# Performance work log

Hardware: AMD Instinct MI355X
Metric: run time of the kernel (lower is better)

The kernel has to match this reference:

```python
import jax, jax.numpy as jnp
import numpy as np

N = 50000
E = 800000
F_IN, F_HID, F_OUT = 128, 64, 40


def setup_inputs() -> dict:
    key = jax.random.key(0)
    ks = jax.random.split(key, 8)
    x = jax.random.normal(ks[0], (N, F_IN), dtype=jnp.float32)
    edge_index = jax.random.randint(ks[1], (2, E), 0, N, dtype=jnp.int64)
    # Glorot-style init like PyG GCNConv.lin; stored as [in, out]
    def glorot(k, fi, fo):
        s = jnp.sqrt(6.0 / (fi + fo)).astype(jnp.float32)
        return jax.random.uniform(k, (fi, fo), jnp.float32, -s, s)
    W1 = glorot(ks[2], F_IN, F_HID)
    b1 = jnp.zeros((F_HID,), jnp.float32)
    W2 = glorot(ks[3], F_HID, F_HID)
    b2 = jnp.zeros((F_HID,), jnp.float32)
    W3 = glorot(ks[4], F_HID, F_OUT)
    b3 = jnp.zeros((F_OUT,), jnp.float32)
    return {"x": x, "edge_index": edge_index, "W1": W1, "b1": b1,
            "W2": W2, "b2": b2, "W3": W3, "b3": b3}


def _prep_edges(edge_index):
    # add self-loops, compute symmetric GCN normalization (as PyG gcn_norm)
    loops = jnp.arange(N, dtype=edge_index.dtype)
    src = jnp.concatenate([edge_index[0], loops])
    dst = jnp.concatenate([edge_index[1], loops])
    deg = jax.ops.segment_sum(jnp.ones_like(dst, dtype=jnp.float32), dst,
                              num_segments=N)
    dinv = jnp.where(deg > 0, jax.lax.rsqrt(deg), 0.0)
    norm = dinv[src] * dinv[dst]  # [E+N]
    return src, dst, norm


def _gcn_conv(x, W, b, src, dst, norm):
    h = x @ W                                  # [N, out] dense projection
    msg = h[src] * norm[:, None]               # gather + scale, [E+N, out]
    out = jax.ops.segment_sum(msg, dst, num_segments=N)  # scatter-add
    return out + b


def reference(x, edge_index, W1, b1, W2, b2, W3, b3):
    src, dst, norm = _prep_edges(edge_index)
    h = jax.nn.relu(_gcn_conv(x, W1, b1, src, dst, norm))
    h = jax.nn.relu(_gcn_conv(h, W2, b2, src, dst, norm))
    return _gcn_conv(h, W3, b3, src, dst, norm)
```

## Files before the change

### kernel.cpp

```cpp
#include <hip/hip_runtime.h>
#include <hip/hip_fp16.h>
#include <math.h>

#define NN 50000
#define EE 800000
#define FIN 128
#define FHID 64
#define FOUT 40

#define BSH  6
#define NBKT ((NN + 63) >> 6)
#define CAP  1600
#define KBBLK 128
#define CHK  (EE / KBBLK)


__global__ void k_detect(const unsigned int* __restrict__ w, int* __restrict__ flag,
                         int* __restrict__ gcur) {
    int t = threadIdx.x;
    if (t < NBKT) gcur[t] = t * CAP;
    if (t == 0) *flag = 1;
    __syncthreads();
    unsigned v = w[2 * t + 1];
    unsigned long long b = __ballot(v != 0);
    if (b && (t & 63) == 0) atomicAnd(flag, 0);
}


__global__ __launch_bounds__(256) void k_bucket(const unsigned int* __restrict__ w,
                                                const int* __restrict__ flag,
                                                int* __restrict__ gcur,
                                                unsigned int* __restrict__ BKT) {
    __shared__ int hist[NBKT], rsv[NBKT], lcur[NBKT];
    const int tid = threadIdx.x;
    for (int i = tid; i < NBKT; i += 256) { hist[i] = 0; lcur[i] = 0; }
    __syncthreads();
    const bool f64 = (*flag) != 0;
    const int e0 = blockIdx.x * CHK, e1 = e0 + CHK;

    for (int e = e0 + tid; e < e1; e += 256) {
        unsigned d = f64 ? w[2 * (EE + e)] : w[EE + e];
        atomicAdd(&hist[d >> BSH], 1);
    }
    __syncthreads();
    for (int i = tid; i < NBKT; i += 256) {
        int h = hist[i];
        rsv[i] = h ? atomicAdd(&gcur[i], h) : 0;
    }
    __syncthreads();
    for (int e = e0 + tid; e < e1; e += 256) {
        unsigned s, d;
        if (f64) { s = w[2 * e]; d = w[2 * (EE + e)]; }
        else     { s = w[e];     d = w[EE + e]; }
        unsigned b = d >> BSH;
        int idx = atomicAdd(&lcur[b], 1);
        BKT[rsv[b] + idx] = (d << 16) | s;
    }
}

__global__ __launch_bounds__(256) void k_fine(const unsigned int* __restrict__ BKT,
                                              const int* __restrict__ gcur,
                                              int* __restrict__ off,
                                              float* __restrict__ dinv,
                                              unsigned short* __restrict__ ebuf) {
    __shared__ unsigned st[CAP];
    __shared__ int h[64], sc[64], lc[64];
    __shared__ int red[4];
    const int tid  = threadIdx.x;
    const int lane = tid & 63;
    const int wid  = tid >> 6;
    const int b    = blockIdx.x;

    int partial = 0;
    for (int i = tid; i < b; i += 256) partial += gcur[i] - i * CAP;
#pragma unroll
    for (int o = 1; o < 64; o <<= 1) partial += __shfl_xor(partial, o, 64);
    if (lane == 0) red[wid] = partial;
    if (tid < 64) { h[tid] = 0; lc[tid] = 0; }
    __syncthreads();
    const int bb = red[0] + red[1] + red[2] + red[3];

    int cnt = gcur[b] - b * CAP;
    if (cnt > CAP) cnt = CAP;
    for (int i = tid; i < cnt; i += 256) {
        unsigned p = BKT[b * CAP + i];
        st[i] = p;
        atomicAdd(&h[(p >> 16) & 63], 1);
    }
    __syncthreads();
    if (tid < 64) {
        int v = h[tid];
        int incl = v;
#pragma unroll
        for (int o = 1; o < 64; o <<= 1) {
            int u = __shfl_up(incl, o, 64);
            if (tid >= o) incl += u;
        }
        sc[tid] = incl - v;
        int n = (b << BSH) + tid;
        if (n < NN) {
            off[n]  = bb + sc[tid];
            dinv[n] = 1.0f / sqrtf((float)(v + 1));
        }
    }
    if (b == 0 && tid == 64) off[NN] = EE;
    __syncthreads();
    for (int i = tid; i < cnt; i += 256) {
        unsigned p = st[i];
        int l = (p >> 16) & 63;
        int idx = atomicAdd(&lc[l], 1);
        ebuf[bb + sc[l] + idx] = (unsigned short)(p & 0xffffu);
    }
}


__global__ __launch_bounds__(256) void k_gemm1(const float* __restrict__ X,
                                               const float* __restrict__ W,
                                               const float* __restrict__ dinv,
                                               unsigned short* __restrict__ Ph) {
    constexpr int K = FIN, ROWS = 16, XP = K + 4;
    __shared__ float Ws[K * 64];
    __shared__ float Xs[ROWS * XP];
    const int tid  = threadIdx.x;
    const int row0 = blockIdx.x * ROWS;
    const int row_end = (NN - row0 < ROWS) ? (NN - row0) : ROWS;

    for (int i = tid; i < K * 16; i += 256)
        ((float4*)Ws)[i] = ((const float4*)W)[i];
    for (int i = tid; i < row_end * (K / 4); i += 256) {
        int r = i / (K / 4), c = i % (K / 4);
        float4 v = ((const float4*)X)[(size_t)(row0 + r) * (K / 4) + c];
        *(float4*)&Xs[r * XP + 4 * c] = v;
    }
    __syncthreads();

    const int r  = tid >> 4;
    const int cg = tid & 15;
    const int grow = row0 + r;
    if (r >= row_end) return;

    float a0 = 0.f, a1 = 0.f, a2 = 0.f, a3 = 0.f;
#pragma unroll 4
    for (int k = 0; k < K; k++) {
        float xv = Xs[r * XP + k];
        float4 wv = *(const float4*)&Ws[k * 64 + cg * 4];
        a0 = fmaf(xv, wv.x, a0);
        a1 = fmaf(xv, wv.y, a1);
        a2 = fmaf(xv, wv.z, a2);
        a3 = fmaf(xv, wv.w, a3);
    }
    float dv = dinv[grow];
    ushort4 o;
    o.x = __half_as_ushort(__float2half_rn(a0 * dv));
    o.y = __half_as_ushort(__float2half_rn(a1 * dv));
    o.z = __half_as_ushort(__float2half_rn(a2 * dv));
    o.w = __half_as_ushort(__float2half_rn(a3 * dv));
    *(ushort4*)&Ph[(size_t)grow * 64 + cg * 4] = o;
}


__device__ __forceinline__ void acc_h(float4& acc, uint2 u) {
    __half2 h01 = *reinterpret_cast<const __half2*>(&u.x);
    __half2 h23 = *reinterpret_cast<const __half2*>(&u.y);
    acc.x += __low2float(h01);
    acc.y += __high2float(h01);
    acc.z += __low2float(h23);
    acc.w += __high2float(h23);
}

__device__ __forceinline__ float4 gather_row_sum(const uint2* __restrict__ Pu,
                                                 const unsigned short* __restrict__ ebuf,
                                                 int node, int s, int e, int g, int q) {
    float4 acc = {0.f, 0.f, 0.f, 0.f};
    if (g == 0) acc_h(acc, Pu[(size_t)node * 16 + q]);
    int i = s;
    for (; i + 15 < e; i += 16) {
        int c0 = ebuf[i + g], c1 = ebuf[i + g + 4], c2 = ebuf[i + g + 8], c3 = ebuf[i + g + 12];
        uint2 u0 = Pu[(size_t)c0 * 16 + q];
        uint2 u1 = Pu[(size_t)c1 * 16 + q];
        uint2 u2 = Pu[(size_t)c2 * 16 + q];
        uint2 u3 = Pu[(size_t)c3 * 16 + q];
        acc_h(acc, u0); acc_h(acc, u1); acc_h(acc, u2); acc_h(acc, u3);
    }
    if (i < e) {
        int j0 = i + g, j1 = i + g + 4, j2 = i + g + 8, j3 = i + g + 12;
        uint2 u0 = Pu[(size_t)ebuf[j0 < e ? j0 : e - 1] * 16 + q];
        uint2 u1 = Pu[(size_t)ebuf[j1 < e ? j1 : e - 1] * 16 + q];
        uint2 u2 = Pu[(size_t)ebuf[j2 < e ? j2 : e - 1] * 16 + q];
        uint2 u3 = Pu[(size_t)ebuf[j3 < e ? j3 : e - 1] * 16 + q];
        if (j0 < e) acc_h(acc, u0);
        if (j1 < e) acc_h(acc, u1);
        if (j2 < e) acc_h(acc, u2);
        if (j3 < e) acc_h(acc, u3);
    }
#pragma unroll
    for (int o = 16; o <= 32; o <<= 1) {
        acc.x += __shfl_xor(acc.x, o, 64);
        acc.y += __shfl_xor(acc.y, o, 64);
        acc.z += __shfl_xor(acc.z, o, 64);
        acc.w += __shfl_xor(acc.w, o, 64);
    }
    return acc;
}


__global__ __launch_bounds__(256) void k_agg1(const uint2* __restrict__ Pu,
                                              const int* __restrict__ off,
                                              const unsigned short* __restrict__ ebuf,
                                              const float* __restrict__ dinv,
                                              const float4* __restrict__ bias4,
                                              unsigned short* __restrict__ HA) {
    const int gid  = blockIdx.x * blockDim.x + threadIdx.x;
    const int node = gid >> 6;
    const int lane = threadIdx.x & 63;
    if (node >= NN) return;
    const int g = lane >> 4, q = lane & 15;
    float4 acc = gather_row_sum(Pu, ebuf, node, off[node], off[node + 1], g, q);
    if (lane < 16) {
        float dv = dinv[node];
        float4 b = bias4[q];
        float4 v;
        v.x = fmaxf(fmaf(acc.x, dv, b.x), 0.f) * dv;
        v.y = fmaxf(fmaf(acc.y, dv, b.y), 0.f) * dv;
        v.z = fmaxf(fmaf(acc.z, dv, b.z), 0.f) * dv;
        v.w = fmaxf(fmaf(acc.w, dv, b.w), 0.f) * dv;
        ushort4 o;
        o.x = __half_as_ushort(__float2half_rn(v.x));
        o.y = __half_as_ushort(__float2half_rn(v.y));
        o.z = __half_as_ushort(__float2half_rn(v.z));
        o.w = __half_as_ushort(__float2half_rn(v.w));
        ((ushort4*)HA)[(size_t)node * 16 + q] = o;
    }
}


template <int MOUT, bool OUTF16>
__global__ __launch_bounds__(256) void k_fuse(const uint2* __restrict__ Hu,
                                              const float* __restrict__ W,
                                              const int* __restrict__ off,
                                              const unsigned short* __restrict__ ebuf,
                                              const float* __restrict__ dinv,
                                              const float* __restrict__ bias,
                                              void* __restrict__ outv) {
    __shared__ float Ws[64 * MOUT];
    __shared__ float aggL[4 * 64];
    const int tid  = threadIdx.x;
    const int lane = tid & 63;
    const int wv   = tid >> 6;
    const int g = lane >> 4, q = lane & 15;

    for (int i = tid; i < 64 * MOUT / 4; i += 256)
        ((float4*)Ws)[i] = ((const float4*)W)[i];
    __syncthreads();

    const float bv = (lane < MOUT) ? bias[lane] : 0.f;
    const int n0 = blockIdx.x * 16 + wv * 4;

#pragma unroll 1
    for (int j = 0; j < 4; j++) {
        const int node = n0 + j;
        float4 acc = gather_row_sum(Hu, ebuf, node, off[node], off[node + 1], g, q);
        const float dv = dinv[node];
        if (lane < 16) {
            float4 t;
            t.x = acc.x * dv; t.y = acc.y * dv; t.z = acc.z * dv; t.w = acc.w * dv;
            *(float4*)&aggL[wv * 64 + q * 4] = t;
        }
        if (lane < MOUT) {
            float o = 0.f;
#pragma unroll 8
            for (int k = 0; k < 64; k++)
                o = fmaf(aggL[wv * 64 + k], Ws[k * MOUT + lane], o);
            float v = o + bv;
            if constexpr (OUTF16) {
                v = fmaxf(v, 0.f);
                ((unsigned short*)outv)[(size_t)node * 64 + lane] =
                    __half_as_ushort(__float2half_rn(v * dv));
            } else {
                ((float*)outv)[(size_t)node * MOUT + lane] = v;
            }
        }
    }
}


static inline size_t alignup(size_t x) { return (x + 255) & ~(size_t)255; }

extern "C" void kernel_launch(void* const* d_in, const int* in_sizes, int n_in,
                              void* d_out, int out_size, void* d_ws, size_t ws_size,
                              hipStream_t stream) {
    const float*        x  = (const float*)d_in[0];
    const unsigned int* ew = (const unsigned int*)d_in[1];
    const float*        W1 = (const float*)d_in[2];
    const float*        b1 = (const float*)d_in[3];
    const float*        W2 = (const float*)d_in[4];
    const float*        b2 = (const float*)d_in[5];
    const float*        W3 = (const float*)d_in[6];
    const float*        b3 = (const float*)d_in[7];

    char* w = (char*)d_ws;
    int*            flag = (int*)w;            w += alignup(4);
    int*            gcur = (int*)w;            w += alignup(NBKT * 4);
    int*            off  = (int*)w;            w += alignup((NN + 1) * 4);
    float*          dinv = (float*)w;          w += alignup(NN * 4);
    unsigned int*   BKT  = (unsigned int*)w;   w += alignup((size_t)NBKT * CAP * 4);
    unsigned short* ebuf = (unsigned short*)w; w += alignup(EE * 2);
    unsigned short* Ph   = (unsigned short*)w; w += alignup((size_t)NN * 64 * 2);
    unsigned short* HA   = (unsigned short*)w; w += alignup((size_t)NN * 64 * 2);
    unsigned short* HB   = (unsigned short*)w; w += alignup((size_t)NN * 64 * 2);

    const int BA = (NN * 64) / 256;
    const int BG = (NN + 15) / 16;

    k_detect<<<1, 1024, 0, stream>>>(ew, flag, gcur);
    k_bucket<<<KBBLK, 256, 0, stream>>>(ew, flag, gcur, BKT);
    k_fine<<<NBKT, 256, 0, stream>>>(BKT, gcur, off, dinv, ebuf);

    k_gemm1<<<BG, 256, 0, stream>>>(x, W1, dinv, Ph);
    k_agg1<<<BA, 256, 0, stream>>>((const uint2*)Ph, off, ebuf, dinv,
                                   (const float4*)b1, HA);

    k_fuse<FHID, true><<<BG, 256, 0, stream>>>((const uint2*)HA, W2, off, ebuf,
                                               dinv, b2, HB);

    k_fuse<FOUT, false><<<BG, 256, 0, stream>>>((const uint2*)HB, W3, off, ebuf,
                                                dinv, b3, d_out);
}
```

Before: 220.6 us.

## Widen gather loads to 16-byte rows and use one wave per node in fused layers

```diff
diff --git a/kernel.cpp b/kernel.cpp
--- a/kernel.cpp
+++ b/kernel.cpp
@@ -159,126 +159,134 @@
 }
 
 
-__device__ __forceinline__ void acc_h(float4& acc, uint2 u) {
+__device__ __forceinline__ void acc_h8(float4& A, float4& B, uint4 u) {
     __half2 h01 = *reinterpret_cast<const __half2*>(&u.x);
     __half2 h23 = *reinterpret_cast<const __half2*>(&u.y);
-    acc.x += __low2float(h01);
-    acc.y += __high2float(h01);
-    acc.z += __low2float(h23);
-    acc.w += __high2float(h23);
-}
-
-__device__ __forceinline__ float4 gather_row_sum(const uint2* __restrict__ Pu,
-                                                 const unsigned short* __restrict__ ebuf,
-                                                 int node, int s, int e, int g, int q) {
-    float4 acc = {0.f, 0.f, 0.f, 0.f};
-    if (g == 0) acc_h(acc, Pu[(size_t)node * 16 + q]);
+    __half2 h45 = *reinterpret_cast<const __half2*>(&u.z);
+    __half2 h67 = *reinterpret_cast<const __half2*>(&u.w);
+    A.x += __low2float(h01); A.y += __high2float(h01);
+    A.z += __low2float(h23); A.w += __high2float(h23);
+    B.x += __low2float(h45); B.y += __high2float(h45);
+    B.z += __low2float(h67); B.w += __high2float(h67);
+}
+
+__device__ __forceinline__ void gather_row_sum8(const uint4* __restrict__ Pu,
+                                                const unsigned short* __restrict__ ebuf,
+                                                int node, int s, int e, int g, int q,
+                                                float4& A, float4& B) {
+    A = {0.f, 0.f, 0.f, 0.f};
+    B = {0.f, 0.f, 0.f, 0.f};
+    if (g == 0) acc_h8(A, B, Pu[(size_t)node * 8 + q]);
     int i = s;
     for (; i + 15 < e; i += 16) {
-        int c0 = ebuf[i + g], c1 = ebuf[i + g + 4], c2 = ebuf[i + g + 8], c3 = ebuf[i + g + 12];
-        uint2 u0 = Pu[(size_t)c0 * 16 + q];
-        uint2 u1 = Pu[(size_t)c1 * 16 + q];
-        uint2 u2 = Pu[(size_t)c2 * 16 + q];
-        uint2 u3 = Pu[(size_t)c3 * 16 + q];
-        acc_h(acc, u0); acc_h(acc, u1); acc_h(acc, u2); acc_h(acc, u3);
+        int c0 = ebuf[i + g], c1 = ebuf[i + g + 8];
+        uint4 u0 = Pu[(size_t)c0 * 8 + q];
+        uint4 u1 = Pu[(size_t)c1 * 8 + q];
+        acc_h8(A, B, u0); acc_h8(A, B, u1);
     }
     if (i < e) {
-        int j0 = i + g, j1 = i + g + 4, j2 = i + g + 8, j3 = i + g + 12;
-        uint2 u0 = Pu[(size_t)ebuf[j0 < e ? j0 : e - 1] * 16 + q];
-        uint2 u1 = Pu[(size_t)ebuf[j1 < e ? j1 : e - 1] * 16 + q];
-        uint2 u2 = Pu[(size_t)ebuf[j2 < e ? j2 : e - 1] * 16 + q];
-        uint2 u3 = Pu[(size_t)ebuf[j3 < e ? j3 : e - 1] * 16 + q];
-        if (j0 < e) acc_h(acc, u0);
-        if (j1 < e) acc_h(acc, u1);
-        if (j2 < e) acc_h(acc, u2);
-        if (j3 < e) acc_h(acc, u3);
+        int j0 = i + g, j1 = i + g + 8;
+        uint4 u0 = Pu[(size_t)ebuf[j0 < e ? j0 : e - 1] * 8 + q];
+        uint4 u1 = Pu[(size_t)ebuf[j1 < e ? j1 : e - 1] * 8 + q];
+        if (j0 < e) acc_h8(A, B, u0);
+        if (j1 < e) acc_h8(A, B, u1);
     }
 #pragma unroll
-    for (int o = 16; o <= 32; o <<= 1) {
-        acc.x += __shfl_xor(acc.x, o, 64);
-        acc.y += __shfl_xor(acc.y, o, 64);
-        acc.z += __shfl_xor(acc.z, o, 64);
-        acc.w += __shfl_xor(acc.w, o, 64);
-    }
-    return acc;
-}
-
-
-__global__ __launch_bounds__(256) void k_agg1(const uint2* __restrict__ Pu,
+    for (int o = 8; o <= 32; o <<= 1) {
+        A.x += __shfl_xor(A.x, o, 64); A.y += __shfl_xor(A.y, o, 64);
+        A.z += __shfl_xor(A.z, o, 64); A.w += __shfl_xor(A.w, o, 64);
+        B.x += __shfl_xor(B.x, o, 64); B.y += __shfl_xor(B.y, o, 64);
+        B.z += __shfl_xor(B.z, o, 64); B.w += __shfl_xor(B.w, o, 64);
+    }
+}
+
+__device__ __forceinline__ uint4 pack8(float4 A, float4 B) {
+    uint4 o;
+    o.x = (unsigned)__half_as_ushort(__float2half_rn(A.x)) |
+          ((unsigned)__half_as_ushort(__float2half_rn(A.y)) << 16);
+    o.y = (unsigned)__half_as_ushort(__float2half_rn(A.z)) |
+          ((unsigned)__half_as_ushort(__float2half_rn(A.w)) << 16);
+    o.z = (unsigned)__half_as_ushort(__float2half_rn(B.x)) |
+          ((unsigned)__half_as_ushort(__float2half_rn(B.y)) << 16);
+    o.w = (unsigned)__half_as_ushort(__float2half_rn(B.z)) |
+          ((unsigned)__half_as_ushort(__float2half_rn(B.w)) << 16);
+    return o;
+}
+
+
+__global__ __launch_bounds__(256) void k_agg1(const uint4* __restrict__ Pu,
                                               const int* __restrict__ off,
                                               const unsigned short* __restrict__ ebuf,
                                               const float* __restrict__ dinv,
-                                              const float4* __restrict__ bias4,
-                                              unsigned short* __restrict__ HA) {
+                                              const float* __restrict__ bias,
+                                              uint4* __restrict__ HA) {
     const int gid  = blockIdx.x * blockDim.x + threadIdx.x;
     const int node = gid >> 6;
     const int lane = threadIdx.x & 63;
     if (node >= NN) return;
-    const int g = lane >> 4, q = lane & 15;
-    float4 acc = gather_row_sum(Pu, ebuf, node, off[node], off[node + 1], g, q);
-    if (lane < 16) {
+    const int g = lane >> 3, q = lane & 7;
+    float4 A, B;
+    gather_row_sum8(Pu, ebuf, node, off[node], off[node + 1], g, q, A, B);
+    if (lane < 8) {
         float dv = dinv[node];
-        float4 b = bias4[q];
-        float4 v;
-        v.x = fmaxf(fmaf(acc.x, dv, b.x), 0.f) * dv;
-        v.y = fmaxf(fmaf(acc.y, dv, b.y), 0.f) * dv;
-        v.z = fmaxf(fmaf(acc.z, dv, b.z), 0.f) * dv;
-        v.w = fmaxf(fmaf(acc.w, dv, b.w), 0.f) * dv;
-        ushort4 o;
-        o.x = __half_as_ushort(__float2half_rn(v.x));
-        o.y = __half_as_ushort(__float2half_rn(v.y));
-        o.z = __half_as_ushort(__float2half_rn(v.z));
-        o.w = __half_as_ushort(__float2half_rn(v.w));
-        ((ushort4*)HA)[(size_t)node * 16 + q] = o;
+        const float4 b0 = *(const float4*)&bias[q * 8];
+        const float4 b1 = *(const float4*)&bias[q * 8 + 4];
+        float4 VA, VB;
+        VA.x = fmaxf(fmaf(A.x, dv, b0.x), 0.f) * dv;
+        VA.y = fmaxf(fmaf(A.y, dv, b0.y), 0.f) * dv;
+        VA.z = fmaxf(fmaf(A.z, dv, b0.z), 0.f) * dv;
+        VA.w = fmaxf(fmaf(A.w, dv, b0.w), 0.f) * dv;
+        VB.x = fmaxf(fmaf(B.x, dv, b1.x), 0.f) * dv;
+        VB.y = fmaxf(fmaf(B.y, dv, b1.y), 0.f) * dv;
+        VB.z = fmaxf(fmaf(B.z, dv, b1.z), 0.f) * dv;
+        VB.w = fmaxf(fmaf(B.w, dv, b1.w), 0.f) * dv;
+        HA[(size_t)node * 8 + q] = pack8(VA, VB);
     }
 }
 
 
 template <int MOUT, bool OUTF16>
-__global__ __launch_bounds__(256) void k_fuse(const uint2* __restrict__ Hu,
-                                              const float* __restrict__ W,
-                                              const int* __restrict__ off,
-                                              const unsigned short* __restrict__ ebuf,
-                                              const float* __restrict__ dinv,
-                                              const float* __restrict__ bias,
-                                              void* __restrict__ outv) {
+__global__ __launch_bounds__(1024) void k_fuse(const uint4* __restrict__ Hu,
+                                               const float* __restrict__ W,
+                                               const int* __restrict__ off,
+                                               const unsigned short* __restrict__ ebuf,
+                                               const float* __restrict__ dinv,
+                                               const float* __restrict__ bias,
+                                               void* __restrict__ outv) {
     __shared__ float Ws[64 * MOUT];
-    __shared__ float aggL[4 * 64];
+    __shared__ float aggL[16 * 64];
     const int tid  = threadIdx.x;
     const int lane = tid & 63;
     const int wv   = tid >> 6;
-    const int g = lane >> 4, q = lane & 15;
-
-    for (int i = tid; i < 64 * MOUT / 4; i += 256)
+    const int g = lane >> 3, q = lane & 7;
+
+    for (int i = tid; i < 64 * MOUT / 4; i += 1024)
         ((float4*)Ws)[i] = ((const float4*)W)[i];
     __syncthreads();
 
-    const float bv = (lane < MOUT) ? bias[lane] : 0.f;
-    const int n0 = blockIdx.x * 16 + wv * 4;
-
-#pragma unroll 1
-    for (int j = 0; j < 4; j++) {
-        const int node = n0 + j;
-        float4 acc = gather_row_sum(Hu, ebuf, node, off[node], off[node + 1], g, q);
-        const float dv = dinv[node];
-        if (lane < 16) {
-            float4 t;
-            t.x = acc.x * dv; t.y = acc.y * dv; t.z = acc.z * dv; t.w = acc.w * dv;
-            *(float4*)&aggL[wv * 64 + q * 4] = t;
-        }
-        if (lane < MOUT) {
-            float o = 0.f;
+    const int node = blockIdx.x * 16 + wv;
+    float4 A, B;
+    gather_row_sum8(Hu, ebuf, node, off[node], off[node + 1], g, q, A, B);
+    const float dv = dinv[node];
+    if (lane < 8) {
+        float4 t0, t1;
+        t0.x = A.x * dv; t0.y = A.y * dv; t0.z = A.z * dv; t0.w = A.w * dv;
+        t1.x = B.x * dv; t1.y = B.y * dv; t1.z = B.z * dv; t1.w = B.w * dv;
+        *(float4*)&aggL[wv * 64 + q * 8]     = t0;
+        *(float4*)&aggL[wv * 64 + q * 8 + 4] = t1;
+    }
+    if (lane < MOUT) {
+        float o = 0.f;
 #pragma unroll 8
-            for (int k = 0; k < 64; k++)
-                o = fmaf(aggL[wv * 64 + k], Ws[k * MOUT + lane], o);
-            float v = o + bv;
-            if constexpr (OUTF16) {
-                v = fmaxf(v, 0.f);
-                ((unsigned short*)outv)[(size_t)node * 64 + lane] =
-                    __half_as_ushort(__float2half_rn(v * dv));
-            } else {
-                ((float*)outv)[(size_t)node * MOUT + lane] = v;
-            }
+        for (int k = 0; k < 64; k++)
+            o = fmaf(aggL[wv * 64 + k], Ws[k * MOUT + lane], o);
+        float v = o + bias[lane];
+        if constexpr (OUTF16) {
+            v = fmaxf(v, 0.f);
+            ((unsigned short*)outv)[(size_t)node * 64 + lane] =
+                __half_as_ushort(__float2half_rn(v * dv));
+        } else {
+            ((float*)outv)[(size_t)node * MOUT + lane] = v;
         }
     }
 }
@@ -317,12 +325,12 @@
     k_fine<<<NBKT, 256, 0, stream>>>(BKT, gcur, off, dinv, ebuf);
 
     k_gemm1<<<BG, 256, 0, stream>>>(x, W1, dinv, Ph);
-    k_agg1<<<BA, 256, 0, stream>>>((const uint2*)Ph, off, ebuf, dinv,
-                                   (const float4*)b1, HA);
-
-    k_fuse<FHID, true><<<BG, 256, 0, stream>>>((const uint2*)HA, W2, off, ebuf,
-                                               dinv, b2, HB);
-
-    k_fuse<FOUT, false><<<BG, 256, 0, stream>>>((const uint2*)HB, W3, off, ebuf,
-                                                dinv, b3, d_out);
-}
+    k_agg1<<<BA, 256, 0, stream>>>((const uint4*)Ph, off, ebuf, dinv, b1,
+                                   (uint4*)HA);
+
+    k_fuse<FHID, true><<<BG, 1024, 0, stream>>>((const uint4*)HA, W2, off, ebuf,
+                                                dinv, b2, HB);
+
+    k_fuse<FOUT, false><<<BG, 1024, 0, stream>>>((const uint4*)HB, W3, off, ebuf,
+                                                 dinv, b3, d_out);
+}
```

Measured after the change: 247.6 us. 1.12x slower.
